# Kernel tuning notes

Measured on AMD Instinct MI355X. Metric: run time of the kernel, lower is better.

## Reference

```python
import jax, jax.numpy as jnp
import numpy as np

N_NODES = 100000
N_EDGES = 1250000
D_FEAT = 64


def setup_inputs() -> dict:
    key = jax.random.key(0)
    k1, k2 = jax.random.split(key)
    x = jax.random.normal(k1, (N_NODES, D_FEAT), dtype=jnp.float32)
    edge_index = jax.random.randint(k2, (2, N_EDGES), 0, N_NODES, dtype=jnp.int64)
    return {"t": 0, "x": x, "edge_index": edge_index}


def reference(t, x, edge_index):
    # LGConv(normalize=False): out[i] = sum_{(j->i) in E} x[j]
    # adj_t SpMM expressed as gather + segment-sum scatter.
    src = edge_index[0]  # source/neighbor nodes
    dst = edge_index[1]  # destination nodes
    msgs = x[src]  # [E, D] gather
    out = jax.ops.segment_sum(msgs, dst, num_segments=N_NODES)  # [N, D]
    return out
```

## Files before the change

### kernel.cpp

```cpp
#include <hip/hip_runtime.h>

#define N_NODES 100000
#define N_EDGES 1250000
#define D_FEAT 64

#define NB_SHIFT 7
#define NODES_PER_B 128
#define N_BUCKETS ((N_NODES + NODES_PER_B - 1) / NODES_PER_B)
#define TROW (N_BUCKETS + 1)
#define NB_PAD 1024
#define MAX_BUCKET_EDGES 2048
#define SRC_BITS 17
#define SRC_MASK ((1u << SRC_BITS) - 1u)

#define CH 4992
#define NCH ((N_EDGES + CH - 1) / CH)
#define NCHP 256

#define NR 4
#define RANGE_SZ 25000u
#define NKEY (NODES_PER_B * NR)

typedef float f32x4 __attribute__((ext_vector_type(4)));

__global__ __launch_bounds__(256) void lgconv_scatter(
    const float* __restrict__ x, const int* __restrict__ src,
    const int* __restrict__ dst, float* __restrict__ out) {
    int tid  = blockIdx.x * blockDim.x + threadIdx.x;
    int edge = tid >> 4;
    int f4   = (tid & 15) << 2;
    if (edge >= N_EDGES) return;
    int s = src[edge], d = dst[edge];
    const float4 v = *reinterpret_cast<const float4*>(x + (size_t)s * D_FEAT + f4);
    float* o = out + (size_t)d * D_FEAT + f4;
    unsafeAtomicAdd(o + 0, v.x); unsafeAtomicAdd(o + 1, v.y);
    unsafeAtomicAdd(o + 2, v.z); unsafeAtomicAdd(o + 3, v.w);
}

__device__ __forceinline__ unsigned short f2bf(float f) {
    unsigned int u = __float_as_uint(f);
    return (unsigned short)((u + 0x7FFFu + ((u >> 16) & 1u)) >> 16);
}
__device__ __forceinline__ float bflo(unsigned int p) {
    return __uint_as_float(p << 16);
}
__device__ __forceinline__ float bfhi(unsigned int p) {
    return __uint_as_float(p & 0xFFFF0000u);
}

__device__ __forceinline__ int wscan_incl(int v) {
    const int lane = threadIdx.x & 63;
#pragma unroll
    for (int off = 1; off < 64; off <<= 1) {
        int u = __shfl_up(v, off, 64);
        if (lane >= off) v += u;
    }
    return v;
}

template <bool CONV>
__global__ __launch_bounds__(1024) void k1_sort(
    const float* __restrict__ x, unsigned short* __restrict__ xb,
    const int* __restrict__ src, const int* __restrict__ dst,
    unsigned int* __restrict__ bins, unsigned short* __restrict__ tableT) {
    __shared__ int hist[NB_PAD];
    __shared__ int scanBase[NB_PAD];
    __shared__ int cur[NB_PAD];
    __shared__ int wsum[16];
    __shared__ unsigned int stage[CH];
    const int t    = threadIdx.x;
    const int c    = blockIdx.x;
    const int base = c * CH;
    const int cnt  = min(CH, N_EDGES - base);
    const int lane = t & 63;
    const int wid  = t >> 6;

    if (CONV) {
        const int F4 = N_NODES * D_FEAT / 4;
        for (int i = c * 1024 + t; i < F4; i += NCH * 1024) {
            float4 v = reinterpret_cast<const float4*>(x)[i];
            ushort4 o;
            o.x = f2bf(v.x); o.y = f2bf(v.y); o.z = f2bf(v.z); o.w = f2bf(v.w);
            reinterpret_cast<ushort4*>(xb)[i] = o;
        }
    }

    hist[t] = 0; cur[t] = 0;
    __syncthreads();
    for (int i = t; i < cnt; i += 1024)
        atomicAdd(&hist[dst[base + i] >> NB_SHIFT], 1);
    __syncthreads();

    int v = hist[t];
    int s = wscan_incl(v);
    if (lane == 63) wsum[wid] = s;
    __syncthreads();
    if (t < 16) {
        int w  = wsum[t];
        wsum[t] = wscan_incl(w);
    }
    __syncthreads();
    int incl = s + (wid ? wsum[wid - 1] : 0);
    scanBase[t] = incl - v;
    __syncthreads();

    if (t < TROW) tableT[(size_t)t * NCHP + c] = (unsigned short)scanBase[t];

    for (int i = t; i < cnt; i += 1024) {
        int d = dst[base + i], sv = src[base + i];
        int b = d >> NB_SHIFT;
        unsigned int packed = ((unsigned int)(d & (NODES_PER_B - 1)) << SRC_BITS)
                            | (unsigned int)sv;
        int pos = scanBase[b] + atomicAdd(&cur[b], 1);
        stage[pos] = packed;
    }
    __syncthreads();
    for (int i = t; i < cnt; i += 1024) bins[base + i] = stage[i];
}

template <bool BF>
__global__ __launch_bounds__(512) void k2_accum(
    const float* __restrict__ x, const unsigned short* __restrict__ xb,
    const unsigned int* __restrict__ bins, const unsigned short* __restrict__ tableT,
    float* __restrict__ out) {
    __shared__ int            startA[512];
    __shared__ unsigned short lenA[512];
    __shared__ int            destB[512];
    __shared__ unsigned int   raw[MAX_BUCKET_EDGES];
    __shared__ unsigned int   srcs[MAX_BUCKET_EDGES];
    __shared__ int cntArr[NKEY];
    __shared__ int nodeOff[NKEY + 1];
    __shared__ int curN[NKEY];
    __shared__ int wsum[8];
    const int t    = threadIdx.x;
    const int b    = blockIdx.x;
    const int lane = t & 63;
    const int wid  = t >> 6;

    int st = 0, len = 0;
    if (t < NCH) {
        st  = __builtin_nontemporal_load(tableT + (size_t)b * NCHP + t);
        len = (int)__builtin_nontemporal_load(tableT + (size_t)(b + 1) * NCHP + t) - st;
    }
    startA[t] = st;
    lenA[t]   = (unsigned short)len;
    cntArr[t] = 0;
    int s = wscan_incl(len);
    if (lane == 63) wsum[wid] = s;
    __syncthreads();
    if (t < 8) {
        int w  = wsum[t];
        wsum[t] = wscan_incl(w);
    }
    __syncthreads();
    int incl = s + (wid ? wsum[wid - 1] : 0);
    destB[t] = incl - len;
    int cntTot = wsum[7];
    if (cntTot > MAX_BUCKET_EDGES) cntTot = MAX_BUCKET_EDGES;
    __syncthreads();

    {
        const int cj = t >> 3;
        const int jj = t & 7;
        for (int c0 = 0; c0 < NCH; c0 += 64) {
            int c = c0 + cj;
            if (c < NCH) {
                int l = lenA[c], s0 = startA[c], db = destB[c];
                const unsigned int* p = bins + (size_t)c * CH + s0;
                for (int q = jj; q < l; q += 8)
                    raw[db + q] = __builtin_nontemporal_load(p + q);
            }
        }
    }
    __syncthreads();

    for (int i = t; i < cntTot; i += 512) {
        unsigned int p = raw[i];
        int key = ((p >> SRC_BITS) << 2) | ((p & SRC_MASK) / RANGE_SZ);
        atomicAdd(&cntArr[key], 1);
    }
    __syncthreads();
    int v2 = cntArr[t];
    int s2 = wscan_incl(v2);
    if (lane == 63) wsum[wid] = s2;
    __syncthreads();
    if (t < 8) {
        int w  = wsum[t];
        wsum[t] = wscan_incl(w);
    }
    __syncthreads();
    int excl = s2 + (wid ? wsum[wid - 1] : 0) - v2;
    nodeOff[t] = excl;
    curN[t]    = excl;
    if (t == 0) nodeOff[NKEY] = cntTot;
    __syncthreads();
    for (int i = t; i < cntTot; i += 512) {
        unsigned int p = raw[i];
        int key = ((p >> SRC_BITS) << 2) | ((p & SRC_MASK) / RANGE_SZ);
        int pos = atomicAdd(&curN[key], 1);
        srcs[pos] = p & SRC_MASK;
    }
    __syncthreads();

    if (BF) {
        const int f0  = (t & 7) << 3;
        const int sub = t >> 3;
        float a0=0,a1=0,a2=0,a3=0,a4=0,a5=0,a6=0,a7=0;
        float b0=0,b1=0,b2=0,b3=0,b4=0,b5=0,b6=0,b7=0;
        for (int r = 0; r < NR; ++r) {
            {
                int idx = (sub << 2) | r;
                int k = nodeOff[idx], end = nodeOff[idx + 1];
                for (; k + 1 < end; k += 2) {
                    const uint4 u0 = *reinterpret_cast<const uint4*>(
                        xb + (size_t)srcs[k] * D_FEAT + f0);
                    const uint4 u1 = *reinterpret_cast<const uint4*>(
                        xb + (size_t)srcs[k + 1] * D_FEAT + f0);
                    a0 += bflo(u0.x) + bflo(u1.x);
                    a1 += bfhi(u0.x) + bfhi(u1.x);
                    a2 += bflo(u0.y) + bflo(u1.y);
                    a3 += bfhi(u0.y) + bfhi(u1.y);
                    a4 += bflo(u0.z) + bflo(u1.z);
                    a5 += bfhi(u0.z) + bfhi(u1.z);
                    a6 += bflo(u0.w) + bflo(u1.w);
                    a7 += bfhi(u0.w) + bfhi(u1.w);
                }
                if (k < end) {
                    const uint4 u = *reinterpret_cast<const uint4*>(
                        xb + (size_t)srcs[k] * D_FEAT + f0);
                    a0 += bflo(u.x); a1 += bfhi(u.x);
                    a2 += bflo(u.y); a3 += bfhi(u.y);
                    a4 += bflo(u.z); a5 += bfhi(u.z);
                    a6 += bflo(u.w); a7 += bfhi(u.w);
                }
            }
            {
                int idx = ((64 + sub) << 2) | r;
                int k = nodeOff[idx], end = nodeOff[idx + 1];
                for (; k + 1 < end; k += 2) {
                    const uint4 u0 = *reinterpret_cast<const uint4*>(
                        xb + (size_t)srcs[k] * D_FEAT + f0);
                    const uint4 u1 = *reinterpret_cast<const uint4*>(
                        xb + (size_t)srcs[k + 1] * D_FEAT + f0);
                    b0 += bflo(u0.x) + bflo(u1.x);
                    b1 += bfhi(u0.x) + bfhi(u1.x);
                    b2 += bflo(u0.y) + bflo(u1.y);
                    b3 += bfhi(u0.y) + bfhi(u1.y);
                    b4 += bflo(u0.z) + bflo(u1.z);
                    b5 += bfhi(u0.z) + bfhi(u1.z);
                    b6 += bflo(u0.w) + bflo(u1.w);
                    b7 += bfhi(u0.w) + bfhi(u1.w);
                }
                if (k < end) {
                    const uint4 u = *reinterpret_cast<const uint4*>(
                        xb + (size_t)srcs[k] * D_FEAT + f0);
                    b0 += bflo(u.x); b1 += bfhi(u.x);
                    b2 += bflo(u.y); b3 += bfhi(u.y);
                    b4 += bflo(u.z); b5 += bfhi(u.z);
                    b6 += bflo(u.w); b7 += bfhi(u.w);
                }
            }
            __syncthreads();
        }
        {
            int node = b * NODES_PER_B + sub;
            if (node < N_NODES) {
                float* op = out + (size_t)node * D_FEAT + f0;
                f32x4 w0 = {a0, a1, a2, a3};
                f32x4 w1 = {a4, a5, a6, a7};
                __builtin_nontemporal_store(w0, reinterpret_cast<f32x4*>(op));
                __builtin_nontemporal_store(w1, reinterpret_cast<f32x4*>(op + 4));
            }
            node = b * NODES_PER_B + 64 + sub;
            if (node < N_NODES) {
                float* op = out + (size_t)node * D_FEAT + f0;
                f32x4 w0 = {b0, b1, b2, b3};
                f32x4 w1 = {b4, b5, b6, b7};
                __builtin_nontemporal_store(w0, reinterpret_cast<f32x4*>(op));
                __builtin_nontemporal_store(w1, reinterpret_cast<f32x4*>(op + 4));
            }
        }
    } else {
        int lane4 = (t & 15) << 2;
        for (int g = 0; g < NODES_PER_B / 32; ++g) {
            int local = g * 32 + (t >> 4);
            int node  = b * NODES_PER_B + local;
            int beg = nodeOff[local << 2], end = nodeOff[(local << 2) + 4];
            float4 acc = make_float4(0.f, 0.f, 0.f, 0.f);
            int k = beg;
            for (; k + 1 < end; k += 2) {
                unsigned int i0 = srcs[k], i1 = srcs[k + 1];
                const float4 a = *reinterpret_cast<const float4*>(x + (size_t)i0 * D_FEAT + lane4);
                const float4 c = *reinterpret_cast<const float4*>(x + (size_t)i1 * D_FEAT + lane4);
                acc.x += a.x + c.x; acc.y += a.y + c.y;
                acc.z += a.z + c.z; acc.w += a.w + c.w;
            }
            if (k < end) {
                unsigned int i0 = srcs[k];
                const float4 a = *reinterpret_cast<const float4*>(x + (size_t)i0 * D_FEAT + lane4);
                acc.x += a.x; acc.y += a.y; acc.z += a.z; acc.w += a.w;
            }
            if (node < N_NODES)
                *reinterpret_cast<float4*>(out + (size_t)node * D_FEAT + lane4) = acc;
        }
    }
}

extern "C" void kernel_launch(void* const* d_in, const int* in_sizes, int n_in,
                              void* d_out, int out_size, void* d_ws, size_t ws_size,
                              hipStream_t stream) {
    const float* x   = (const float*)d_in[1];
    const int*   ei  = (const int*)d_in[2];
    const int*   src = ei;
    const int*   dst = ei + N_EDGES;
    float*       out = (float*)d_out;

    const size_t tabBytes = (size_t)TROW * NCHP * sizeof(unsigned short);
    const size_t binBytes = (size_t)N_EDGES * sizeof(unsigned int);
    const size_t xbOff    = (binBytes + tabBytes + 15) & ~(size_t)15;
    const size_t needA    = xbOff + (size_t)N_NODES * D_FEAT * sizeof(unsigned short);
    const size_t needB    = binBytes + tabBytes;

    if (ws_size >= needA) {
        unsigned int*   bins   = (unsigned int*)d_ws;
        unsigned short* tableT = (unsigned short*)((char*)d_ws + binBytes);
        unsigned short* xb     = (unsigned short*)((char*)d_ws + xbOff);
        k1_sort<true><<<NCH, 1024, 0, stream>>>(x, xb, src, dst, bins, tableT);
        k2_accum<true><<<N_BUCKETS, 512, 0, stream>>>(x, xb, bins, tableT, out);
    } else if (ws_size >= needB) {
        unsigned int*   bins   = (unsigned int*)d_ws;
        unsigned short* tableT = (unsigned short*)((char*)d_ws + binBytes);
        k1_sort<false><<<NCH, 1024, 0, stream>>>(x, nullptr, src, dst, bins, tableT);
        k2_accum<false><<<N_BUCKETS, 512, 0, stream>>>(x, nullptr, bins, tableT, out);
    } else {
        (void)hipMemsetAsync(out, 0, (size_t)out_size * sizeof(float), stream);
        const int total = N_EDGES * 16;
        lgconv_scatter<<<(total + 255) / 256, 256, 0, stream>>>(x, src, dst, out);
    }
}
```

Before: 123.9 us.

## Halve sort chunk size, use 512-thread blocks with register-held edges

The first kernel now processes half-size edge chunks with 512-thread blocks. Each thread loads its five edges into registers once instead of reading dst/src twice, and the bucket scan covers two bins per thread. This doubles the number of chunks, so the chunk table is widened and the second kernel's gather loop is retuned to four threads per chunk across 128 chunks per pass. The goal is more resident blocks and fewer global reloads in the sort pass. The cost is more, shorter per-bucket segments for the accumulate kernel to gather.

Result: slower. 130.2 us (+5.0%).

```diff
diff --git a/kernel.cpp b/kernel.cpp
--- a/kernel.cpp
+++ b/kernel.cpp
@@ -13,9 +13,11 @@
 #define SRC_BITS 17
 #define SRC_MASK ((1u << SRC_BITS) - 1u)
 
-#define CH 4992
+#define BLK1 512
+#define CH 2496
 #define NCH ((N_EDGES + CH - 1) / CH)
-#define NCHP 256
+#define NCHP 512
+#define EPT 5
 
 #define NR 4
 #define RANGE_SZ 25000u
@@ -59,14 +61,14 @@
 }
 
 template <bool CONV>
-__global__ __launch_bounds__(1024) void k1_sort(
+__global__ __launch_bounds__(BLK1, 4) void k1_sort(
     const float* __restrict__ x, unsigned short* __restrict__ xb,
     const int* __restrict__ src, const int* __restrict__ dst,
     unsigned int* __restrict__ bins, unsigned short* __restrict__ tableT) {
     __shared__ int hist[NB_PAD];
     __shared__ int scanBase[NB_PAD];
     __shared__ int cur[NB_PAD];
-    __shared__ int wsum[16];
+    __shared__ int wsum[BLK1 / 64];
     __shared__ unsigned int stage[CH];
     const int t    = threadIdx.x;
     const int c    = blockIdx.x;
@@ -77,7 +79,7 @@
 
     if (CONV) {
         const int F4 = N_NODES * D_FEAT / 4;
-        for (int i = c * 1024 + t; i < F4; i += NCH * 1024) {
+        for (int i = c * BLK1 + t; i < F4; i += NCH * BLK1) {
             float4 v = reinterpret_cast<const float4*>(x)[i];
             ushort4 o;
             o.x = f2bf(v.x); o.y = f2bf(v.y); o.z = f2bf(v.z); o.w = f2bf(v.w);
@@ -85,37 +87,56 @@
         }
     }
 
-    hist[t] = 0; cur[t] = 0;
-    __syncthreads();
-    for (int i = t; i < cnt; i += 1024)
-        atomicAdd(&hist[dst[base + i] >> NB_SHIFT], 1);
-    __syncthreads();
-
-    int v = hist[t];
-    int s = wscan_incl(v);
+    hist[t] = 0; hist[t + BLK1] = 0;
+    cur[t]  = 0; cur[t + BLK1]  = 0;
+    __syncthreads();
+
+    int rd[EPT], rs[EPT];
+#pragma unroll
+    for (int r = 0; r < EPT; ++r) {
+        int i = t + r * BLK1;
+        if (i < cnt) {
+            rd[r] = dst[base + i];
+            rs[r] = src[base + i];
+            atomicAdd(&hist[rd[r] >> NB_SHIFT], 1);
+        } else {
+            rd[r] = -1;
+        }
+    }
+    __syncthreads();
+
+    int v0 = hist[2 * t], v1 = hist[2 * t + 1];
+    int pv = v0 + v1;
+    int s  = wscan_incl(pv);
     if (lane == 63) wsum[wid] = s;
     __syncthreads();
-    if (t < 16) {
+    if (t < BLK1 / 64) {
         int w  = wsum[t];
         wsum[t] = wscan_incl(w);
     }
     __syncthreads();
     int incl = s + (wid ? wsum[wid - 1] : 0);
-    scanBase[t] = incl - v;
-    __syncthreads();
-
-    if (t < TROW) tableT[(size_t)t * NCHP + c] = (unsigned short)scanBase[t];
-
-    for (int i = t; i < cnt; i += 1024) {
-        int d = dst[base + i], sv = src[base + i];
-        int b = d >> NB_SHIFT;
-        unsigned int packed = ((unsigned int)(d & (NODES_PER_B - 1)) << SRC_BITS)
-                            | (unsigned int)sv;
-        int pos = scanBase[b] + atomicAdd(&cur[b], 1);
-        stage[pos] = packed;
-    }
-    __syncthreads();
-    for (int i = t; i < cnt; i += 1024) bins[base + i] = stage[i];
+    int eb   = incl - pv;
+    scanBase[2 * t]     = eb;
+    scanBase[2 * t + 1] = eb + v0;
+    __syncthreads();
+
+    for (int i = t; i < TROW; i += BLK1)
+        tableT[(size_t)i * NCHP + c] = (unsigned short)scanBase[i];
+
+#pragma unroll
+    for (int r = 0; r < EPT; ++r) {
+        if (rd[r] >= 0) {
+            int b = rd[r] >> NB_SHIFT;
+            unsigned int packed =
+                ((unsigned int)(rd[r] & (NODES_PER_B - 1)) << SRC_BITS)
+                | (unsigned int)rs[r];
+            int pos = scanBase[b] + atomicAdd(&cur[b], 1);
+            stage[pos] = packed;
+        }
+    }
+    __syncthreads();
+    for (int i = t; i < cnt; i += BLK1) bins[base + i] = stage[i];
 }
 
 template <bool BF>
@@ -160,14 +181,14 @@
     __syncthreads();
 
     {
-        const int cj = t >> 3;
-        const int jj = t & 7;
-        for (int c0 = 0; c0 < NCH; c0 += 64) {
+        const int cj = t >> 2;
+        const int jj = t & 3;
+        for (int c0 = 0; c0 < NCH; c0 += 128) {
             int c = c0 + cj;
             if (c < NCH) {
                 int l = lenA[c], s0 = startA[c], db = destB[c];
                 const unsigned int* p = bins + (size_t)c * CH + s0;
-                for (int q = jj; q < l; q += 8)
+                for (int q = jj; q < l; q += 4)
                     raw[db + q] = __builtin_nontemporal_load(p + q);
             }
         }
@@ -325,12 +346,12 @@
         unsigned int*   bins   = (unsigned int*)d_ws;
         unsigned short* tableT = (unsigned short*)((char*)d_ws + binBytes);
         unsigned short* xb     = (unsigned short*)((char*)d_ws + xbOff);
-        k1_sort<true><<<NCH, 1024, 0, stream>>>(x, xb, src, dst, bins, tableT);
+        k1_sort<true><<<NCH, BLK1, 0, stream>>>(x, xb, src, dst, bins, tableT);
         k2_accum<true><<<N_BUCKETS, 512, 0, stream>>>(x, xb, bins, tableT, out);
     } else if (ws_size >= needB) {
         unsigned int*   bins   = (unsigned int*)d_ws;
         unsigned short* tableT = (unsigned short*)((char*)d_ws + binBytes);
-        k1_sort<false><<<NCH, 1024, 0, stream>>>(x, nullptr, src, dst, bins, tableT);
+        k1_sort<false><<<NCH, BLK1, 0, stream>>>(x, nullptr, src, dst, bins, tableT);
         k2_accum<false><<<N_BUCKETS, 512, 0, stream>>>(x, nullptr, bins, tableT, out);
     } else {
         (void)hipMemsetAsync(out, 0, (size_t)out_size * sizeof(float), stream);
```
